# Kernel optimization log

Measured on AMD Instinct MI355X. Metric: run time of the kernel, lower is better.

The kernel has to match this reference:

```python
import jax, jax.numpy as jnp
import numpy as np

N = 8192      # sequence length (rows of query/key/value)
D = 768       # model dim (Conv1d in_channels)
DFF = 2048    # FFN hidden dim (Conv1d out_channels)


def setup_inputs() -> dict:
    key = jax.random.key(0)
    ks = jax.random.split(key, 7)
    query = jax.random.normal(ks[0], (N, D), dtype=jnp.float32)
    k = jax.random.normal(ks[1], (N, D), dtype=jnp.float32)
    value = jax.random.normal(ks[2], (N, D), dtype=jnp.float32)
    # Conv1d(kernel_size=1) == dense layer: weight [out,in], bias [out]
    W1 = jax.random.normal(ks[3], (DFF, D), dtype=jnp.float32) * 0.02
    b1 = jax.random.normal(ks[4], (DFF,), dtype=jnp.float32) * 0.02
    W2 = jax.random.normal(ks[5], (D, DFF), dtype=jnp.float32) * 0.02
    b2 = jax.random.normal(ks[6], (D,), dtype=jnp.float32) * 0.02
    return {"query": query, "key": k, "value": value,
            "W1": W1, "b1": b1, "W2": W2, "b2": b2}


def reference(query, key, value, W1, b1, W2, b2):
    # manual attention: no 1/sqrt(d) scaling in the original module
    scores = jnp.matmul(query, key.T)              # [N, N]
    attn = jax.nn.softmax(scores, axis=-1)         # [N, N]
    context = jnp.matmul(attn, value)              # [N, D]
    # conv1x1 -> ReLU -> conv1x1 (2-layer MLP)
    h = jax.nn.relu(jnp.matmul(context, W1.T) + b1)  # [N, DFF]
    out = jnp.matmul(h, W2.T) + b2                   # [N, D]
    return out
```

## Files before the change

kernel.cpp:

```cpp
#include <hip/hip_runtime.h>
#include <cstdint>
#include <cstddef>

#define DEV __device__ __forceinline__

typedef _Float16 f16;
typedef __attribute__((ext_vector_type(8))) _Float16 f16x8;
typedef __attribute__((ext_vector_type(4))) float f32x4;
typedef __attribute__((ext_vector_type(4))) unsigned short us4;

DEV unsigned short f2h(float f) {
  f16 h = (f16)f;
  return __builtin_bit_cast(unsigned short, h);
}

DEV void async_ld16(const void* g, void* l) {
  __builtin_amdgcn_global_load_lds(
      (__attribute__((address_space(1))) unsigned int*)(uintptr_t)g,
      (__attribute__((address_space(3))) unsigned int*)(uint32_t)(uintptr_t)l,
      16, 0, 0);
}

#define MFMA16(d, a, b_) (d) = __builtin_amdgcn_mfma_f32_16x16x32_f16((a), (b_), (d), 0, 0, 0)

template <int BN, int EPI, bool RELU, bool HASBIAS, bool ALPHA, bool XCD>
__global__ __launch_bounds__(512, 2) void gemm256(
    const unsigned short* __restrict__ A, const unsigned short* __restrict__ B,
    void* __restrict__ Cp, const float* __restrict__ bias,
    const unsigned short* __restrict__ alp, int Mtot,
    int K, int lda, int ldb, int ldc, int nt, int mt, int sl) {
  extern __shared__ char smem[];
  constexpr int FN = BN / 64;
  constexpr int WCW = BN / 4;
  constexpr int BUFSZ = 32768 + BN * 128;
  const int NT = K >> 6;

  int mb, nb, zb;
  {
    const int b = blockIdx.x;
    if (XCD) {
      const int xcd = b & 7, q = b >> 3;
      nb = q % nt;
      const int rest = q / nt;
      zb = rest % sl;
      mb = xcd * (mt >> 3) + rest / sl;
    } else {
      nb = b % nt;
      const int t = b / nt;
      mb = t % mt;
      zb = t / mt;
    }
  }
  const int bm = mb << 8, bn = nb * BN;
  const unsigned koff = (unsigned)zb * (unsigned)K;

  const int tid = threadIdx.x;
  const int wave = tid >> 6, lane = tid & 63;
  const int wr = wave >> 2, wc = wave & 3;
  const int mr = lane & 15, quad = lane >> 4;

  const int slot = tid & 7, rr = tid >> 3;
  const int ce = (slot ^ (rr & 7)) << 3;

  f32x4 acc[8][FN] = {};
  f16x8 av0[4][2], av1[4][2], bv0[2][2], bv1[FN - 2][2];
  const f16* alb = (const f16*)(smem + 2 * BUFSZ);

  if (ALPHA) {
    const int ntl = K >> 7;
    const unsigned short* g0 = alp + (size_t)(zb * ntl) * Mtot + bm;
    uint4* s = (uint4*)(smem + 2 * BUFSZ);
    const int nu4 = (ntl << 5);
    for (int idx = tid; idx < nu4; idx += 512) {
      const int tt = idx >> 5;
      const int ru = (idx & 31) << 3;
      s[idx] = *(const uint4*)(g0 + (size_t)tt * Mtot + ru);
    }
  }

  auto stA = [&](int h, int Ts) {
    const int t_ = Ts >= NT ? Ts - NT : Ts;
    const unsigned kk = koff + (unsigned)(t_ << 6);
    char* l = smem + (Ts & 1) * BUFSZ + h * 16384 + wave * 1024;
#pragma unroll
    for (int p = 0; p < 2; ++p) {
      const unsigned off = (unsigned)(bm + p * 128 + h * 64 + rr) * (unsigned)lda + kk + ce;
      async_ld16(A + off, l + p * 8192);
    }
  };
  auto stB = [&](int h, int Ts) {
    const int t_ = Ts >= NT ? Ts - NT : Ts;
    const unsigned kk = koff + (unsigned)(t_ << 6);
    char* l = smem + (Ts & 1) * BUFSZ + 32768 + h * 16384 + wave * 1024;
    if (BN == 256) {
#pragma unroll
      for (int p = 0; p < 2; ++p) {
        const int g = bn + p * 128 + (rr >> 5) * 64 + h * 32 + (rr & 31);
        async_ld16(B + ((unsigned)g * (unsigned)ldb + kk + ce), l + p * 8192);
      }
    } else if (h == 0) {
#pragma unroll
      for (int p = 0; p < 2; ++p) {
        const int g = bn + (p * 2 + (rr >> 5)) * 48 + (rr & 31);
        async_ld16(B + ((unsigned)g * (unsigned)ldb + kk + ce), l + p * 8192);
      }
    } else {
      const int g = bn + (rr >> 4) * 48 + 32 + (rr & 15);
      async_ld16(B + ((unsigned)g * (unsigned)ldb + kk + ce), l);
    }
  };
  auto rdA = [&](int bufc, int i, int ks) {
    const int r = wr * 64 + (i & 3) * 16 + mr;
    return *(const f16x8*)(smem + bufc + (i >> 2) * 16384 + r * 128 +
                           ((((ks << 2) | quad) ^ (mr & 7)) << 4));
  };
  auto rdB0 = [&](int bufc, int j, int ks) {
    const int rb = wc * 32 + j * 16 + mr;
    return *(const f16x8*)(smem + bufc + 32768 + rb * 128 +
                           ((((ks << 2) | quad) ^ (mr & 7)) << 4));
  };
  auto rdB1 = [&](int bufc, int j, int ks) {
    const int rb = (BN == 256) ? (wc * 32 + (j - 2) * 16 + mr) : (wc * 16 + mr);
    return *(const f16x8*)(smem + bufc + 32768 + 16384 + rb * 128 +
                           ((((ks << 2) | quad) ^ (mr & 7)) << 4));
  };

  stA(0, 0); stB(0, 0); stA(1, 0); stB(1, 0);
  stA(0, 1); stB(0, 1); stA(1, 1);
  if (ALPHA) asm volatile("s_waitcnt lgkmcnt(0)" ::: "memory");
  asm volatile("s_waitcnt vmcnt(6)" ::: "memory");
  __builtin_amdgcn_s_barrier();

  for (int T = 0; T < NT; ++T) {
    const int bufc = (T & 1) * BUFSZ;
    f16 a0_[4], a1_[4];
#pragma unroll
    for (int i = 0; i < 4; ++i) { av0[i][0] = rdA(bufc, i, 0); av0[i][1] = rdA(bufc, i, 1); }
    if (ALPHA) {
#pragma unroll
      for (int i = 0; i < 4; ++i) a0_[i] = alb[(T >> 1) * 256 + wr * 128 + i * 16 + mr];
    }
    stB(1, T + 1);
    __builtin_amdgcn_s_barrier();
    asm volatile("s_waitcnt lgkmcnt(0)" ::: "memory");
    __builtin_amdgcn_sched_barrier(0);
    if (ALPHA) {
#pragma unroll
      for (int i = 0; i < 4; ++i) { av0[i][0] = av0[i][0] * a0_[i]; av0[i][1] = av0[i][1] * a0_[i]; }
    }
    if (T) {
      __builtin_amdgcn_s_setprio(1);
#pragma unroll
      for (int i = 0; i < 4; ++i)
#pragma unroll
        for (int j = 0; j < FN - 2; ++j) {
          MFMA16(acc[4 + i][2 + j], av1[i][0], bv1[j][0]);
          MFMA16(acc[4 + i][2 + j], av1[i][1], bv1[j][1]);
        }
      __builtin_amdgcn_s_setprio(0);
    }
    __builtin_amdgcn_s_barrier();
#pragma unroll
    for (int j = 0; j < 2; ++j) { bv0[j][0] = rdB0(bufc, j, 0); bv0[j][1] = rdB0(bufc, j, 1); }
    stA(0, T + 2);
    __builtin_amdgcn_s_barrier();
    asm volatile("s_waitcnt lgkmcnt(0)" ::: "memory");
    __builtin_amdgcn_sched_barrier(0);
    __builtin_amdgcn_s_setprio(1);
#pragma unroll
    for (int i = 0; i < 4; ++i)
#pragma unroll
      for (int j = 0; j < 2; ++j) {
        MFMA16(acc[i][j], av0[i][0], bv0[j][0]);
        MFMA16(acc[i][j], av0[i][1], bv0[j][1]);
      }
    __builtin_amdgcn_s_setprio(0);
    __builtin_amdgcn_s_barrier();
#pragma unroll
    for (int i = 0; i < 4; ++i) { av1[i][0] = rdA(bufc, 4 + i, 0); av1[i][1] = rdA(bufc, 4 + i, 1); }
    if (ALPHA) {
#pragma unroll
      for (int i = 0; i < 4; ++i) a1_[i] = alb[(T >> 1) * 256 + wr * 128 + 64 + i * 16 + mr];
    }
    stB(0, T + 2);
    __builtin_amdgcn_s_barrier();
    asm volatile("s_waitcnt lgkmcnt(0)" ::: "memory");
    __builtin_amdgcn_sched_barrier(0);
    if (ALPHA) {
#pragma unroll
      for (int i = 0; i < 4; ++i) { av1[i][0] = av1[i][0] * a1_[i]; av1[i][1] = av1[i][1] * a1_[i]; }
    }
    __builtin_amdgcn_s_setprio(1);
#pragma unroll
    for (int i = 0; i < 4; ++i)
#pragma unroll
      for (int j = 0; j < 2; ++j) {
        MFMA16(acc[4 + i][j], av1[i][0], bv0[j][0]);
        MFMA16(acc[4 + i][j], av1[i][1], bv0[j][1]);
      }
    __builtin_amdgcn_s_setprio(0);
    __builtin_amdgcn_s_barrier();
#pragma unroll
    for (int j = 0; j < FN - 2; ++j) { bv1[j][0] = rdB1(bufc, 2 + j, 0); bv1[j][1] = rdB1(bufc, 2 + j, 1); }
    stA(1, T + 2);
    __builtin_amdgcn_s_barrier();
    asm volatile("s_waitcnt lgkmcnt(0)" ::: "memory");
    __builtin_amdgcn_sched_barrier(0);
    __builtin_amdgcn_s_setprio(1);
#pragma unroll
    for (int i = 0; i < 4; ++i)
#pragma unroll
      for (int j = 0; j < FN - 2; ++j) {
        MFMA16(acc[i][2 + j], av0[i][0], bv1[j][0]);
        MFMA16(acc[i][2 + j], av0[i][1], bv1[j][1]);
      }
    __builtin_amdgcn_s_setprio(0);
    asm volatile("s_waitcnt vmcnt(6)" ::: "memory");
    __builtin_amdgcn_s_barrier();
  }
  __builtin_amdgcn_s_setprio(1);
#pragma unroll
  for (int i = 0; i < 4; ++i)
#pragma unroll
    for (int j = 0; j < FN - 2; ++j) {
      MFMA16(acc[4 + i][2 + j], av1[i][0], bv1[j][0]);
      MFMA16(acc[4 + i][2 + j], av1[i][1], bv1[j][1]);
    }
  __builtin_amdgcn_s_setprio(0);
  asm volatile("s_waitcnt vmcnt(0)" ::: "memory");
  __builtin_amdgcn_s_barrier();

#pragma unroll
  for (int i = 0; i < 8; ++i) {
#pragma unroll
    for (int j = 0; j < FN; ++j) {
      const int col = bn + wc * WCW + j * 16 + mr;
      float bb = 0.f;
      if (HASBIAS) bb = bias[col];
#pragma unroll
      for (int r = 0; r < 4; ++r) {
        const int row = bm + wr * 128 + i * 16 + quad * 4 + r;
        float v = acc[i][j][r];
        if (HASBIAS) v += bb;
        if (RELU) v = fmaxf(v, 0.f);
        if (EPI == 2)
          atomicAdd(&((float*)Cp)[(size_t)row * ldc + col], v);
        else if (EPI == 1)
          ((float*)Cp)[(size_t)zb * Mtot * ldc + (size_t)row * ldc + col] = v;
        else
          ((unsigned short*)Cp)[(size_t)row * ldc + col] = f2h(v);
      }
    }
  }
}

__global__ __launch_bounds__(512, 2) void qk256(
    const unsigned short* __restrict__ A, const unsigned short* __restrict__ B,
    unsigned short* __restrict__ P, float* __restrict__ stm,
    float* __restrict__ stl, int M, int K, int lda, int ldb, int ldc) {
  extern __shared__ char smem[];
  const int NT = K >> 6;

  const int b = blockIdx.x;
  const int xcd = b & 7, c = b >> 3;
  const int mb = ((c >> 5) << 3) | ((c >> 2) & 7);
  const int nb = (xcd << 2) | (c & 3);
  const int bm = mb << 8, bn = nb << 8;

  const int tid = threadIdx.x;
  const int wave = tid >> 6, lane = tid & 63;
  const int wr = wave >> 2, wc = wave & 3;
  const int mr = lane & 15, quad = lane >> 4;

  const int slot = tid & 7, rr = tid >> 3;
  const int ce = (slot ^ (rr & 7)) << 3;

  f32x4 acc[8][4] = {};
  f16x8 av0[4][2], av1[4][2], bv0[2][2], bv1[2][2];

  auto stA = [&](int h, int Ts) {
    const int t = Ts >= NT ? Ts - NT : Ts;
    const int kk = t << 6;
    char* l = smem + ((Ts & 1) << 16) + h * 16384 + wave * 1024;
#pragma unroll
    for (int p = 0; p < 2; ++p) {
      const unsigned off = (unsigned)(bm + p * 128 + h * 64 + rr) * (unsigned)lda + kk + ce;
      async_ld16(A + off, l + p * 8192);
    }
  };
  auto stB = [&](int h, int Ts) {
    const int t = Ts >= NT ? Ts - NT : Ts;
    const int kk = t << 6;
    char* l = smem + ((Ts & 1) << 16) + 32768 + h * 16384 + wave * 1024;
#pragma unroll
    for (int p = 0; p < 2; ++p) {
      const unsigned off =
          (unsigned)(bn + p * 128 + (rr >> 5) * 64 + h * 32 + (rr & 31)) * (unsigned)ldb + kk + ce;
      async_ld16(B + off, l + p * 8192);
    }
  };
  auto rdA = [&](int bufc, int i, int ks) {
    const int r = wr * 64 + (i & 3) * 16 + mr;
    return *(const f16x8*)(smem + bufc + (i >> 2) * 16384 + r * 128 +
                           ((((ks << 2) | quad) ^ (mr & 7)) << 4));
  };
  auto rdB = [&](int bufc, int j, int ks) {
    const int r = wc * 32 + (j & 1) * 16 + mr;
    return *(const f16x8*)(smem + bufc + 32768 + (j >> 1) * 16384 + r * 128 +
                           ((((ks << 2) | quad) ^ (mr & 7)) << 4));
  };

  stA(0, 0); stB(0, 0); stA(1, 0); stB(1, 0);
  stA(0, 1); stB(0, 1); stA(1, 1);
  asm volatile("s_waitcnt vmcnt(6)" ::: "memory");
  __builtin_amdgcn_s_barrier();

  for (int T = 0; T < NT; ++T) {
    const int bufc = (T & 1) << 16;
#pragma unroll
    for (int i = 0; i < 4; ++i) { av0[i][0] = rdA(bufc, i, 0); av0[i][1] = rdA(bufc, i, 1); }
    stB(1, T + 1);
    __builtin_amdgcn_s_barrier();
    asm volatile("s_waitcnt lgkmcnt(0)" ::: "memory");
    __builtin_amdgcn_sched_barrier(0);
    if (T) {
      __builtin_amdgcn_s_setprio(1);
#pragma unroll
      for (int i = 0; i < 4; ++i)
#pragma unroll
        for (int j = 0; j < 2; ++j) {
          MFMA16(acc[4 + i][2 + j], av1[i][0], bv1[j][0]);
          MFMA16(acc[4 + i][2 + j], av1[i][1], bv1[j][1]);
        }
      __builtin_amdgcn_s_setprio(0);
    }
    __builtin_amdgcn_s_barrier();
#pragma unroll
    for (int j = 0; j < 2; ++j) { bv0[j][0] = rdB(bufc, j, 0); bv0[j][1] = rdB(bufc, j, 1); }
    stA(0, T + 2);
    __builtin_amdgcn_s_barrier();
    asm volatile("s_waitcnt lgkmcnt(0)" ::: "memory");
    __builtin_amdgcn_sched_barrier(0);
    __builtin_amdgcn_s_setprio(1);
#pragma unroll
    for (int i = 0; i < 4; ++i)
#pragma unroll
      for (int j = 0; j < 2; ++j) {
        MFMA16(acc[i][j], av0[i][0], bv0[j][0]);
        MFMA16(acc[i][j], av0[i][1], bv0[j][1]);
      }
    __builtin_amdgcn_s_setprio(0);
    __builtin_amdgcn_s_barrier();
#pragma unroll
    for (int i = 0; i < 4; ++i) { av1[i][0] = rdA(bufc, 4 + i, 0); av1[i][1] = rdA(bufc, 4 + i, 1); }
    stB(0, T + 2);
    __builtin_amdgcn_s_barrier();
    asm volatile("s_waitcnt lgkmcnt(0)" ::: "memory");
    __builtin_amdgcn_sched_barrier(0);
    __builtin_amdgcn_s_setprio(1);
#pragma unroll
    for (int i = 0; i < 4; ++i)
#pragma unroll
      for (int j = 0; j < 2; ++j) {
        MFMA16(acc[4 + i][j], av1[i][0], bv0[j][0]);
        MFMA16(acc[4 + i][j], av1[i][1], bv0[j][1]);
      }
    __builtin_amdgcn_s_setprio(0);
    __builtin_amdgcn_s_barrier();
#pragma unroll
    for (int j = 0; j < 2; ++j) { bv1[j][0] = rdB(bufc, 2 + j, 0); bv1[j][1] = rdB(bufc, 2 + j, 1); }
    stA(1, T + 2);
    __builtin_amdgcn_s_barrier();
    asm volatile("s_waitcnt lgkmcnt(0)" ::: "memory");
    __builtin_amdgcn_sched_barrier(0);
    __builtin_amdgcn_s_setprio(1);
#pragma unroll
    for (int i = 0; i < 4; ++i)
#pragma unroll
      for (int j = 0; j < 2; ++j) {
        MFMA16(acc[i][2 + j], av0[i][0], bv1[j][0]);
        MFMA16(acc[i][2 + j], av0[i][1], bv1[j][1]);
      }
    __builtin_amdgcn_s_setprio(0);
    asm volatile("s_waitcnt vmcnt(6)" ::: "memory");
    __builtin_amdgcn_s_barrier();
  }
  __builtin_amdgcn_s_setprio(1);
#pragma unroll
  for (int i = 0; i < 4; ++i)
#pragma unroll
    for (int j = 0; j < 2; ++j) {
      MFMA16(acc[4 + i][2 + j], av1[i][0], bv1[j][0]);
      MFMA16(acc[4 + i][2 + j], av1[i][1], bv1[j][1]);
    }
  __builtin_amdgcn_s_setprio(0);
  asm volatile("s_waitcnt vmcnt(0)" ::: "memory");
  __builtin_amdgcn_s_barrier();

  float* sred = (float*)smem;
  float* ssum = (float*)(smem + 4096);
  const int hc = wc >> 1;
  float Mh[8][4];

#pragma unroll
  for (int i = 0; i < 8; ++i)
#pragma unroll
    for (int r = 0; r < 4; ++r) {
      float m = acc[i][0][r];
#pragma unroll
      for (int j = 1; j < 4; ++j) m = fmaxf(m, acc[i][j][r]);
      m = fmaxf(m, __shfl_xor(m, 1));
      m = fmaxf(m, __shfl_xor(m, 2));
      m = fmaxf(m, __shfl_xor(m, 4));
      m = fmaxf(m, __shfl_xor(m, 8));
      if (mr == 0) sred[(wr * 128 + i * 16 + quad * 4 + r) * 4 + wc] = m;
    }
  __syncthreads();
#pragma unroll
  for (int i = 0; i < 8; ++i)
#pragma unroll
    for (int r = 0; r < 4; ++r) {
      const int row_l = wr * 128 + i * 16 + quad * 4 + r;
      Mh[i][r] = fmaxf(sred[row_l * 4 + 2 * hc], sred[row_l * 4 + 2 * hc + 1]);
    }
#pragma unroll
  for (int i = 0; i < 8; ++i)
#pragma unroll
    for (int r = 0; r < 4; ++r) {
      const int row_l = wr * 128 + i * 16 + quad * 4 + r;
      float l = 0.f;
#pragma unroll
      for (int j = 0; j < 4; ++j) {
        const float e = __expf(acc[i][j][r] - Mh[i][r]);
        P[(size_t)(bm + row_l) * ldc + (bn + wc * 64 + j * 16 + mr)] = f2h(e);
        l += e;
      }
      l += __shfl_xor(l, 1);
      l += __shfl_xor(l, 2);
      l += __shfl_xor(l, 4);
      l += __shfl_xor(l, 8);
      if (mr == 0) ssum[row_l * 4 + wc] = l;
    }
  __syncthreads();
  if ((wc & 1) == 0 && mr == 0) {
#pragma unroll
    for (int i = 0; i < 8; ++i)
#pragma unroll
      for (int r = 0; r < 4; ++r) {
        const int row_l = wr * 128 + i * 16 + quad * 4 + r;
        const int tile = nb * 2 + hc;
        stm[(size_t)tile * M + bm + row_l] = Mh[i][r];
        stl[(size_t)tile * M + bm + row_l] =
            ssum[row_l * 4 + 2 * hc] + ssum[row_l * 4 + 2 * hc + 1];
      }
  }
}

__global__ __launch_bounds__(256) void combine_alpha(
    const float* __restrict__ stm, const float* __restrict__ stl,
    unsigned short* __restrict__ alp, int ntile, int Mtot) {
  const int row = blockIdx.x * 4 + (threadIdx.x >> 6);
  const int t = threadIdx.x & 63;
  float m = (t < ntile) ? stm[(size_t)t * Mtot + row] : -1e30f;
  float M = m;
#pragma unroll
  for (int o = 1; o < 64; o <<= 1) M = fmaxf(M, __shfl_xor(M, o));
  float l = (t < ntile) ? stl[(size_t)t * Mtot + row] : 0.f;
  float c = l * __expf(m - M);
#pragma unroll
  for (int o = 1; o < 64; o <<= 1) c += __shfl_xor(c, o);
  if (t < ntile) alp[(size_t)t * Mtot + row] = f2h(__expf(m - M) / c);
}

__global__ __launch_bounds__(256) void prep4(
    const float* __restrict__ Q, const float* __restrict__ Km,
    const float* __restrict__ W1, const float* __restrict__ W2,
    unsigned short* __restrict__ qh, unsigned short* __restrict__ kh,
    unsigned short* __restrict__ w1h, unsigned short* __restrict__ w2h,
    int nqk4, int nw4) {
  int i = blockIdx.x * 256 + threadIdx.x;
  if (i >= 2 * nqk4 + 2 * nw4) return;
  const float* src;
  unsigned short* dst;
  int j = i;
  if (j < nqk4) { src = Q; dst = qh; }
  else if ((j -= nqk4) < nqk4) { src = Km; dst = kh; }
  else if ((j -= nqk4) < nw4) { src = W1; dst = w1h; }
  else { j -= nw4; src = W2; dst = w2h; }
  f32x4 v = ((const f32x4*)src)[j];
  us4 r;
#pragma unroll
  for (int k = 0; k < 4; ++k) r[k] = f2h(v[k]);
  ((us4*)dst)[j] = r;
}

__global__ __launch_bounds__(256) void combine2_cvt(const f32x4* __restrict__ a,
                                                    const f32x4* __restrict__ b,
                                                    us4* __restrict__ o, int n4) {
  int i = blockIdx.x * 256 + threadIdx.x;
  if (i < n4) {
    f32x4 va = a[i], vb = b[i];
    us4 r;
#pragma unroll
    for (int j = 0; j < 4; ++j) r[j] = f2h(va[j] + vb[j]);
    o[i] = r;
  }
}

__global__ __launch_bounds__(256) void combine2_bias(const f32x4* __restrict__ a,
                                                     const f32x4* __restrict__ b,
                                                     const float* __restrict__ bias,
                                                     f32x4* __restrict__ o, int n4, int d4) {
  int i = blockIdx.x * 256 + threadIdx.x;
  if (i < n4) {
    f32x4 va = a[i], vb = b[i];
    const int c = (i % d4) * 4;
    f32x4 r;
#pragma unroll
    for (int j = 0; j < 4; ++j) r[j] = va[j] + vb[j] + bias[c + j];
    o[i] = r;
  }
}

__global__ __launch_bounds__(256) void vt_kernel(const float* __restrict__ V,
                                                 unsigned short* __restrict__ vT) {
  __shared__ float t[32][33];
  const int bx = blockIdx.x, by = blockIdx.y;
  const int x = threadIdx.x, y = threadIdx.y;
#pragma unroll
  for (int r = 0; r < 4; ++r)
    t[y + r * 8][x] = V[(size_t)(by * 32 + y + r * 8) * 768 + bx * 32 + x];
  __syncthreads();
#pragma unroll
  for (int r = 0; r < 4; ++r)
    vT[(size_t)(bx * 32 + y + r * 8) * 8192 + by * 32 + x] = f2h(t[x][y + r * 8]);
}

extern "C" void kernel_launch(void* const* d_in, const int* in_sizes, int n_in,
                              void* d_out, int out_size, void* d_ws, size_t ws_size,
                              hipStream_t stream) {
  const int N = 8192, D = 768, DFF = 2048;
  const float* Q  = (const float*)d_in[0];
  const float* Km = (const float*)d_in[1];
  const float* V  = (const float*)d_in[2];
  const float* W1 = (const float*)d_in[3];
  const float* b1 = (const float*)d_in[4];
  const float* W2 = (const float*)d_in[5];
  const float* b2 = (const float*)d_in[6];

  char* w = (char*)d_ws;
  size_t off = 0;
  auto take = [&](size_t bytes) { void* p = w + off; off += bytes; return p; };
  unsigned short* qh   = (unsigned short*)take((size_t)N * D * 2);
  unsigned short* kh   = (unsigned short*)take((size_t)N * D * 2);
  unsigned short* vT   = (unsigned short*)take((size_t)N * D * 2);
  unsigned short* ctx16= (unsigned short*)take((size_t)N * D * 2);
  float*          ctx32= (float*)take((size_t)N * D * 4);
  unsigned short* hb   = (unsigned short*)take((size_t)N * DFF * 2);
  unsigned short* w1h  = (unsigned short*)take((size_t)DFF * D * 2);
  unsigned short* w2h  = (unsigned short*)take((size_t)D * DFF * 2);
  float*          stm  = (float*)take((size_t)64 * N * 4);
  float*          stl  = (float*)take((size_t)64 * N * 4);
  unsigned short* alp  = (unsigned short*)take((size_t)64 * N * 2);
  unsigned short* Pp   = (unsigned short*)take((size_t)N * N * 2);
  float* ctxsh = ctx32;
  float* osh   = (float*)Pp;
  (void)ws_size;

  prep4<<<((2 * N * D + 2 * DFF * D) / 4 + 255) / 256, 256, 0, stream>>>(
      Q, Km, W1, W2, qh, kh, w1h, w2h, N * D / 4, DFF * D / 4);
  vt_kernel<<<dim3(D / 32, N / 32), dim3(32, 8), 0, stream>>>(V, vT);

  {
    hipFuncSetAttribute((const void*)qk256,
                        hipFuncAttributeMaxDynamicSharedMemorySize, 131072);
    qk256<<<(N / 256) * (N / 256), 512, 131072, stream>>>(
        qh, kh, Pp, stm, stl, N, D, D, D, N);
  }
  combine_alpha<<<N / 4, 256, 0, stream>>>(stm, stl, alp, 64, N);

  {
    const int nt = D / 192, mt = N / 256, sl = 2;
    constexpr int BUFSZ = 32768 + 192 * 128;
    const int smem_sz = 2 * BUFSZ + ((N / 2) >> 7) * 256 * 2;
    hipFuncSetAttribute((const void*)gemm256<192, 1, false, false, true, true>,
                        hipFuncAttributeMaxDynamicSharedMemorySize, smem_sz);
    gemm256<192, 1, false, false, true, true><<<nt * mt * sl, 512, smem_sz, stream>>>(
        Pp, vT, ctxsh, nullptr, alp, N,
        N / sl, N, N, D, nt, mt, sl);
  }
  combine2_cvt<<<(N * D / 4 + 255) / 256, 256, 0, stream>>>(
      (const f32x4*)ctxsh, (const f32x4*)(ctxsh + (size_t)N * D), (us4*)ctx16, N * D / 4);

  {
    const int nt = DFF / 256, mt = N / 256;
    hipFuncSetAttribute((const void*)gemm256<256, 0, true, true, false, true>,
                        hipFuncAttributeMaxDynamicSharedMemorySize, 131072);
    gemm256<256, 0, true, true, false, true><<<nt * mt, 512, 131072, stream>>>(
        ctx16, w1h, hb, b1, nullptr, N,
        D, D, D, DFF, nt, mt, 1);
  }
  {
    const int nt = D / 192, mt = N / 256, sl = 2;
    constexpr int BUFSZ = 32768 + 192 * 128;
    hipFuncSetAttribute((const void*)gemm256<192, 1, false, false, false, true>,
                        hipFuncAttributeMaxDynamicSharedMemorySize, 2 * BUFSZ);
    gemm256<192, 1, false, false, false, true><<<nt * mt * sl, 512, 2 * BUFSZ, stream>>>(
        hb, w2h, osh, nullptr, nullptr, N,
        DFF / sl, DFF, DFF, D, nt, mt, sl);
  }
  combine2_bias<<<(N * D / 4 + 255) / 256, 256, 0, stream>>>(
      (const f32x4*)osh, (const f32x4*)(osh + (size_t)N * D), b2,
      (f32x4*)d_out, N * D / 4, D / 4);
}
```

Measured before the change: 480.6 us.

## Shrink QK softmax tile to 256x128 with BK=32 for higher occupancy

```diff
diff --git a/kernel.cpp b/kernel.cpp
--- a/kernel.cpp
+++ b/kernel.cpp
@@ -254,161 +254,122 @@
   }
 }
 
-__global__ __launch_bounds__(512, 2) void qk256(
+__global__ __launch_bounds__(512, 4) void qk256(
     const unsigned short* __restrict__ A, const unsigned short* __restrict__ B,
     unsigned short* __restrict__ P, float* __restrict__ stm,
     float* __restrict__ stl, int M, int K, int lda, int ldb, int ldc) {
   extern __shared__ char smem[];
-  const int NT = K >> 6;
+  const int NT = K >> 5;
+  constexpr int BUFSZ = 24576;
 
   const int b = blockIdx.x;
   const int xcd = b & 7, c = b >> 3;
-  const int mb = ((c >> 5) << 3) | ((c >> 2) & 7);
-  const int nb = (xcd << 2) | (c & 3);
-  const int bm = mb << 8, bn = nb << 8;
+  const int mb = c >> 3;
+  const int nb = (xcd << 3) | (c & 7);
+  const int bm = mb << 8, bn = nb << 7;
 
   const int tid = threadIdx.x;
   const int wave = tid >> 6, lane = tid & 63;
   const int wr = wave >> 2, wc = wave & 3;
   const int mr = lane & 15, quad = lane >> 4;
 
-  const int slot = tid & 7, rr = tid >> 3;
-  const int ce = (slot ^ (rr & 7)) << 3;
-
-  f32x4 acc[8][4] = {};
-  f16x8 av0[4][2], av1[4][2], bv0[2][2], bv1[2][2];
+  const int rr2 = tid >> 2;
+  const int ce = ((tid & 3) ^ (rr2 & 3)) << 3;
+  const int arow = (rr2 >> 6) * 128 + (rr2 & 63);
+
+  f32x4 acc[8][2] = {};
+  f16x8 av0[4], av1[4], bv0, bv1;
 
   auto stA = [&](int h, int Ts) {
     const int t = Ts >= NT ? Ts - NT : Ts;
-    const int kk = t << 6;
-    char* l = smem + ((Ts & 1) << 16) + h * 16384 + wave * 1024;
-#pragma unroll
-    for (int p = 0; p < 2; ++p) {
-      const unsigned off = (unsigned)(bm + p * 128 + h * 64 + rr) * (unsigned)lda + kk + ce;
-      async_ld16(A + off, l + p * 8192);
-    }
-  };
-  auto stB = [&](int h, int Ts) {
+    const int kk = t << 5;
+    char* l = smem + (Ts & 1) * BUFSZ + h * 8192 + wave * 1024;
+    async_ld16(A + ((unsigned)(bm + arow + h * 64) * (unsigned)lda + kk + ce), l);
+  };
+  auto stB = [&](int Ts) {
     const int t = Ts >= NT ? Ts - NT : Ts;
-    const int kk = t << 6;
-    char* l = smem + ((Ts & 1) << 16) + 32768 + h * 16384 + wave * 1024;
-#pragma unroll
-    for (int p = 0; p < 2; ++p) {
-      const unsigned off =
-          (unsigned)(bn + p * 128 + (rr >> 5) * 64 + h * 32 + (rr & 31)) * (unsigned)ldb + kk + ce;
-      async_ld16(B + off, l + p * 8192);
-    }
-  };
-  auto rdA = [&](int bufc, int i, int ks) {
+    const int kk = t << 5;
+    char* l = smem + (Ts & 1) * BUFSZ + 16384 + wave * 1024;
+    async_ld16(B + ((unsigned)(bn + rr2) * (unsigned)ldb + kk + ce), l);
+  };
+  auto rdA = [&](int bufc, int i) {
     const int r = wr * 64 + (i & 3) * 16 + mr;
-    return *(const f16x8*)(smem + bufc + (i >> 2) * 16384 + r * 128 +
-                           ((((ks << 2) | quad) ^ (mr & 7)) << 4));
-  };
-  auto rdB = [&](int bufc, int j, int ks) {
-    const int r = wc * 32 + (j & 1) * 16 + mr;
-    return *(const f16x8*)(smem + bufc + 32768 + (j >> 1) * 16384 + r * 128 +
-                           ((((ks << 2) | quad) ^ (mr & 7)) << 4));
-  };
-
-  stA(0, 0); stB(0, 0); stA(1, 0); stB(1, 0);
-  stA(0, 1); stB(0, 1); stA(1, 1);
-  asm volatile("s_waitcnt vmcnt(6)" ::: "memory");
+    return *(const f16x8*)(smem + bufc + (i >> 2) * 8192 + r * 64 +
+                           ((quad ^ (mr & 3)) << 4));
+  };
+  auto rdB = [&](int bufc, int j) {
+    const int r = wc * 32 + j * 16 + mr;
+    return *(const f16x8*)(smem + bufc + 16384 + r * 64 +
+                           ((quad ^ (mr & 3)) << 4));
+  };
+
+  stA(0, 0); stB(0); stA(1, 0); stA(0, 1); stA(1, 1);
+  asm volatile("s_waitcnt vmcnt(2)" ::: "memory");
   __builtin_amdgcn_s_barrier();
 
   for (int T = 0; T < NT; ++T) {
-    const int bufc = (T & 1) << 16;
-#pragma unroll
-    for (int i = 0; i < 4; ++i) { av0[i][0] = rdA(bufc, i, 0); av0[i][1] = rdA(bufc, i, 1); }
-    stB(1, T + 1);
+    const int bufc = (T & 1) * BUFSZ;
+#pragma unroll
+    for (int i = 0; i < 4; ++i) av0[i] = rdA(bufc, i);
+    stB(T + 1);
     __builtin_amdgcn_s_barrier();
     asm volatile("s_waitcnt lgkmcnt(0)" ::: "memory");
     __builtin_amdgcn_sched_barrier(0);
     if (T) {
       __builtin_amdgcn_s_setprio(1);
 #pragma unroll
-      for (int i = 0; i < 4; ++i)
-#pragma unroll
-        for (int j = 0; j < 2; ++j) {
-          MFMA16(acc[4 + i][2 + j], av1[i][0], bv1[j][0]);
-          MFMA16(acc[4 + i][2 + j], av1[i][1], bv1[j][1]);
-        }
+      for (int i = 0; i < 4; ++i) MFMA16(acc[4 + i][1], av1[i], bv1);
       __builtin_amdgcn_s_setprio(0);
     }
     __builtin_amdgcn_s_barrier();
-#pragma unroll
-    for (int j = 0; j < 2; ++j) { bv0[j][0] = rdB(bufc, j, 0); bv0[j][1] = rdB(bufc, j, 1); }
+    bv0 = rdB(bufc, 0);
     stA(0, T + 2);
     __builtin_amdgcn_s_barrier();
     asm volatile("s_waitcnt lgkmcnt(0)" ::: "memory");
     __builtin_amdgcn_sched_barrier(0);
     __builtin_amdgcn_s_setprio(1);
 #pragma unroll
-    for (int i = 0; i < 4; ++i)
-#pragma unroll
-      for (int j = 0; j < 2; ++j) {
-        MFMA16(acc[i][j], av0[i][0], bv0[j][0]);
-        MFMA16(acc[i][j], av0[i][1], bv0[j][1]);
-      }
+    for (int i = 0; i < 4; ++i) MFMA16(acc[i][0], av0[i], bv0);
     __builtin_amdgcn_s_setprio(0);
     __builtin_amdgcn_s_barrier();
 #pragma unroll
-    for (int i = 0; i < 4; ++i) { av1[i][0] = rdA(bufc, 4 + i, 0); av1[i][1] = rdA(bufc, 4 + i, 1); }
-    stB(0, T + 2);
+    for (int i = 0; i < 4; ++i) av1[i] = rdA(bufc, 4 + i);
     __builtin_amdgcn_s_barrier();
     asm volatile("s_waitcnt lgkmcnt(0)" ::: "memory");
     __builtin_amdgcn_sched_barrier(0);
     __builtin_amdgcn_s_setprio(1);
 #pragma unroll
-    for (int i = 0; i < 4; ++i)
-#pragma unroll
-      for (int j = 0; j < 2; ++j) {
-        MFMA16(acc[4 + i][j], av1[i][0], bv0[j][0]);
-        MFMA16(acc[4 + i][j], av1[i][1], bv0[j][1]);
-      }
+    for (int i = 0; i < 4; ++i) MFMA16(acc[4 + i][0], av1[i], bv0);
     __builtin_amdgcn_s_setprio(0);
     __builtin_amdgcn_s_barrier();
-#pragma unroll
-    for (int j = 0; j < 2; ++j) { bv1[j][0] = rdB(bufc, 2 + j, 0); bv1[j][1] = rdB(bufc, 2 + j, 1); }
+    bv1 = rdB(bufc, 1);
     stA(1, T + 2);
     __builtin_amdgcn_s_barrier();
     asm volatile("s_waitcnt lgkmcnt(0)" ::: "memory");
     __builtin_amdgcn_sched_barrier(0);
     __builtin_amdgcn_s_setprio(1);
 #pragma unroll
-    for (int i = 0; i < 4; ++i)
-#pragma unroll
-      for (int j = 0; j < 2; ++j) {
-        MFMA16(acc[i][2 + j], av0[i][0], bv1[j][0]);
-        MFMA16(acc[i][2 + j], av0[i][1], bv1[j][1]);
-      }
+    for (int i = 0; i < 4; ++i) MFMA16(acc[i][1], av0[i], bv1);
     __builtin_amdgcn_s_setprio(0);
-    asm volatile("s_waitcnt vmcnt(6)" ::: "memory");
+    asm volatile("s_waitcnt vmcnt(2)" ::: "memory");
     __builtin_amdgcn_s_barrier();
   }
   __builtin_amdgcn_s_setprio(1);
 #pragma unroll
-  for (int i = 0; i < 4; ++i)
-#pragma unroll
-    for (int j = 0; j < 2; ++j) {
-      MFMA16(acc[4 + i][2 + j], av1[i][0], bv1[j][0]);
-      MFMA16(acc[4 + i][2 + j], av1[i][1], bv1[j][1]);
-    }
+  for (int i = 0; i < 4; ++i) MFMA16(acc[4 + i][1], av1[i], bv1);
   __builtin_amdgcn_s_setprio(0);
   asm volatile("s_waitcnt vmcnt(0)" ::: "memory");
   __builtin_amdgcn_s_barrier();
 
   float* sred = (float*)smem;
   float* ssum = (float*)(smem + 4096);
-  const int hc = wc >> 1;
   float Mh[8][4];
 
 #pragma unroll
   for (int i = 0; i < 8; ++i)
 #pragma unroll
     for (int r = 0; r < 4; ++r) {
-      float m = acc[i][0][r];
-#pragma unroll
-      for (int j = 1; j < 4; ++j) m = fmaxf(m, acc[i][j][r]);
+      float m = fmaxf(acc[i][0][r], acc[i][1][r]);
       m = fmaxf(m, __shfl_xor(m, 1));
       m = fmaxf(m, __shfl_xor(m, 2));
       m = fmaxf(m, __shfl_xor(m, 4));
@@ -421,7 +382,8 @@
 #pragma unroll
     for (int r = 0; r < 4; ++r) {
       const int row_l = wr * 128 + i * 16 + quad * 4 + r;
-      Mh[i][r] = fmaxf(sred[row_l * 4 + 2 * hc], sred[row_l * 4 + 2 * hc + 1]);
+      Mh[i][r] = fmaxf(fmaxf(sred[row_l * 4], sred[row_l * 4 + 1]),
+                       fmaxf(sred[row_l * 4 + 2], sred[row_l * 4 + 3]));
     }
 #pragma unroll
   for (int i = 0; i < 8; ++i)
@@ -430,9 +392,9 @@
       const int row_l = wr * 128 + i * 16 + quad * 4 + r;
       float l = 0.f;
 #pragma unroll
-      for (int j = 0; j < 4; ++j) {
+      for (int j = 0; j < 2; ++j) {
         const float e = __expf(acc[i][j][r] - Mh[i][r]);
-        P[(size_t)(bm + row_l) * ldc + (bn + wc * 64 + j * 16 + mr)] = f2h(e);
+        P[(size_t)(bm + row_l) * ldc + (bn + wc * 32 + j * 16 + mr)] = f2h(e);
         l += e;
       }
       l += __shfl_xor(l, 1);
@@ -442,16 +404,16 @@
       if (mr == 0) ssum[row_l * 4 + wc] = l;
     }
   __syncthreads();
-  if ((wc & 1) == 0 && mr == 0) {
+  if (wc == 0 && mr == 0) {
 #pragma unroll
     for (int i = 0; i < 8; ++i)
 #pragma unroll
       for (int r = 0; r < 4; ++r) {
         const int row_l = wr * 128 + i * 16 + quad * 4 + r;
-        const int tile = nb * 2 + hc;
-        stm[(size_t)tile * M + bm + row_l] = Mh[i][r];
-        stl[(size_t)tile * M + bm + row_l] =
-            ssum[row_l * 4 + 2 * hc] + ssum[row_l * 4 + 2 * hc + 1];
+        stm[(size_t)nb * M + bm + row_l] = Mh[i][r];
+        stl[(size_t)nb * M + bm + row_l] =
+            ssum[row_l * 4] + ssum[row_l * 4 + 1] +
+            ssum[row_l * 4 + 2] + ssum[row_l * 4 + 3];
       }
   }
 }
@@ -573,8 +535,8 @@
 
   {
     hipFuncSetAttribute((const void*)qk256,
-                        hipFuncAttributeMaxDynamicSharedMemorySize, 131072);
-    qk256<<<(N / 256) * (N / 256), 512, 131072, stream>>>(
+                        hipFuncAttributeMaxDynamicSharedMemorySize, 49152);
+    qk256<<<(N / 256) * (N / 128), 512, 49152, stream>>>(
         qh, kh, Pp, stm, stl, N, D, D, D, N);
   }
   combine_alpha<<<N / 4, 256, 0, stream>>>(stm, stl, alp, 64, N);
```

New measurement: 699.6 us. 45.6% more time.
